# Kernel optimization log

Hardware: AMD Instinct MI355X
Metric: run time of the kernel (lower is better)

The kernel has to match this reference:

```python
import jax, jax.numpy as jnp
import numpy as np
from jax import lax


def _lstm_dir(x, W, U, b, reverse):
    # x: [S, B, in]; W: [4H, in]; U: [4H, H]; b: [4H] (b_ih + b_hh combined)
    if reverse:
        x = x[::-1]
    B = x.shape[1]
    H = U.shape[1]

    def step(carry, xt):
        h, c = carry
        g = xt @ W.T + h @ U.T + b  # [B, 4H], torch gate order i,f,g,o
        i, f, gg, o = jnp.split(g, 4, axis=-1)
        c = jax.nn.sigmoid(f) * c + jax.nn.sigmoid(i) * jnp.tanh(gg)
        h = jax.nn.sigmoid(o) * jnp.tanh(c)
        return (h, c), h

    init = (jnp.zeros((B, H), x.dtype), jnp.zeros((B, H), x.dtype))
    _, hs = lax.scan(step, init, x)
    if reverse:
        hs = hs[::-1]
    return hs  # [S, B, H]


def _bilstm_layer(x, Wih, Whh, b):
    # x: [S, B, in]; Wih: [2, 4H, in]; Whh: [2, 4H, H]; b: [2, 4H]
    fwd = _lstm_dir(x, Wih[0], Whh[0], b[0], False)
    bwd = _lstm_dir(x, Wih[1], Whh[1], b[1], True)
    return jnp.concatenate([fwd, bwd], axis=-1)  # [S, B, 2H]


def _forward(words, chars, emb_table, char_emb_table, char_conv_w, char_conv_b,
             lstm_Wih0, lstm_Whh0, lstm_b0, lstm_Wih1, lstm_Whh1, lstm_b1,
             out_w, out_b):
    B, S = words.shape
    emb = emb_table[words]  # [B, S, E] (dropout = identity in eval)

    # Char CNN: one grouped conv over all B*S positions (replaces the per-position
    # Python loop). NOTE: the original forward discards this (word_features is
    # never used), so it does not affect the returned output -- kept for fidelity.
    ce = char_emb_table[chars]                      # [B, S, W, 25]
    Wl = ce.shape[2]
    x = ce.reshape(B * S, Wl, 25).transpose(0, 2, 1)  # [B*S, 25, W]
    conv = lax.conv_general_dilated(
        x, char_conv_w, (1,), 'VALID',
        dimension_numbers=('NCH', 'OIH', 'NCH'), feature_group_count=25)
    char_feat = jnp.max(conv + char_conv_b[None, :, None], axis=2).reshape(B, S, -1)
    del char_feat  # dead w.r.t. output, exactly as in the original module

    # 2-layer BiLSTM over the word embeddings (all lens == S -> packing is identity)
    h = emb.transpose(1, 0, 2)  # [S, B, E]
    h = _bilstm_layer(h, lstm_Wih0, lstm_Whh0, lstm_b0)
    h = _bilstm_layer(h, lstm_Wih1, lstm_Whh1, lstm_b1)
    lstm_out = h.transpose(1, 0, 2)  # [B, S, 2H]

    # attn_out is computed-but-discarded in the original; output uses lstm_out.
    return jax.nn.sigmoid(lstm_out @ out_w.T + out_b)  # [B, S, n_tags]


def setup_inputs():
    key = jax.random.key(0)
    ks = jax.random.split(key, 14)
    B, S, Wl = 32, 128, 20
    V, E, H, T = 50000, 300, 200, 17
    std = 0.1
    words = jax.random.randint(ks[0], (B, S), 1, V + 2).astype(jnp.int32)
    chars = jax.random.randint(ks[1], (B, S, Wl), 1, 123).astype(jnp.int32)
    lens = jnp.full((B,), S, dtype=jnp.int32)  # full-length sentences
    emb_table = (jax.random.normal(ks[2], (V + 2, E), jnp.float32) * std).at[0].set(0.0)
    char_emb_table = jax.random.normal(ks[3], (123, 25), jnp.float32) * std
    char_conv_w = jax.random.normal(ks[4], (125, 1, 3), jnp.float32) * std  # groups=25
    char_conv_b = jax.random.normal(ks[5], (125,), jnp.float32) * std
    lstm_Wih0 = jax.random.normal(ks[6], (2, 4 * H, E), jnp.float32) * std
    lstm_Whh0 = jax.random.normal(ks[7], (2, 4 * H, H), jnp.float32) * std
    lstm_b0 = jax.random.normal(ks[8], (2, 4 * H), jnp.float32) * std
    lstm_Wih1 = jax.random.normal(ks[9], (2, 4 * H, 2 * H), jnp.float32) * std
    lstm_Whh1 = jax.random.normal(ks[10], (2, 4 * H, H), jnp.float32) * std
    lstm_b1 = jax.random.normal(ks[11], (2, 4 * H), jnp.float32) * std
    out_w = jax.random.normal(ks[12], (T, 2 * H), jnp.float32) * std
    out_b = jax.random.normal(ks[13], (T,), jnp.float32) * std
    return {"words": words, "chars": chars, "lens": lens,
            "emb_table": emb_table, "char_emb_table": char_emb_table,
            "char_conv_w": char_conv_w, "char_conv_b": char_conv_b,
            "lstm_Wih0": lstm_Wih0, "lstm_Whh0": lstm_Whh0, "lstm_b0": lstm_b0,
            "lstm_Wih1": lstm_Wih1, "lstm_Whh1": lstm_Whh1, "lstm_b1": lstm_b1,
            "out_w": out_w, "out_b": out_b}


def reference(words, chars, lens, emb_table, char_emb_table, char_conv_w,
              char_conv_b, lstm_Wih0, lstm_Whh0, lstm_b0, lstm_Wih1, lstm_Whh1,
              lstm_b1, out_w, out_b):
    # lens are all == S, so pack_padded/pad_packed is an identity (no masking).
    return _forward(words, chars, emb_table, char_emb_table, char_conv_w,
                    char_conv_b, lstm_Wih0, lstm_Whh0, lstm_b0,
                    lstm_Wih1, lstm_Whh1, lstm_b1, out_w, out_b)
```

## Files before the change

### kernel.cpp

```cpp
#include <hip/hip_runtime.h>
#include <math.h>

#define SEQ 128
#define BATCH 32
#define EDIM 300
#define HDIM 200
#define G4 800
#define NGATE 1600
#define KC 25
#define NLDS 12
#define CHSTRIDE 6400

#define K0PAD 320
#define K1PAD 416

typedef _Float16 h2t __attribute__((ext_vector_type(2)));
typedef _Float16 f16x8 __attribute__((ext_vector_type(8)));
typedef float f32x4 __attribute__((ext_vector_type(4)));

__device__ __forceinline__ h2t u2h(unsigned v) {
    union { unsigned u; h2t h; } c; c.u = v; return c.h;
}

__device__ __forceinline__ float dot2acc(h2t a, h2t b, float c) {
    return __builtin_amdgcn_fdot2(a, b, c, false);
}

__device__ __forceinline__ float dot8(uint4 u, uint4 h, float acc) {
    acc = dot2acc(u2h(u.x), u2h(h.x), acc);
    acc = dot2acc(u2h(u.y), u2h(h.y), acc);
    acc = dot2acc(u2h(u.z), u2h(h.z), acc);
    acc = dot2acc(u2h(u.w), u2h(h.w), acc);
    return acc;
}

__device__ __forceinline__ float fast_sigmoid(float x) {
    return 1.f / (1.f + __expf(-x));
}
__device__ __forceinline__ float fast_tanh(float x) {
    x = fminf(fmaxf(x, -15.f), 15.f);
    float e = __expf(2.f * x);
    return (e - 1.f) / (e + 1.f);
}

__global__ void k_gather(const int* __restrict__ words,
                         const float* __restrict__ emb,
                         _Float16* __restrict__ X0h)
{
    int row = blockIdx.x;
    int t = row >> 5;
    int b = row & 31;
    int w = words[b * SEQ + t];
    const float* src = emb + (size_t)w * EDIM;
    _Float16* dst = X0h + (size_t)row * K0PAD;
    for (int e = threadIdx.x; e < K0PAD; e += blockDim.x)
        dst[e] = (e < EDIM) ? (_Float16)src[e] : (_Float16)0.f;
}

__global__ void k_castW(const float* __restrict__ W,
                        _Float16* __restrict__ Wh,
                        int N, int K, int Kpad)
{
    int idx = blockIdx.x * blockDim.x + threadIdx.x;
    if (idx >= N * Kpad) return;
    int n = idx / Kpad, k = idx % Kpad;
    Wh[idx] = (k < K) ? (_Float16)W[(size_t)n * K + k] : (_Float16)0.f;
}

__global__ void k_pack(const float* __restrict__ Whh,
                       _Float16* __restrict__ Upk)
{
    int idx = blockIdx.x * blockDim.x + threadIdx.x;
    if (idx >= 2 * KC * 800) return;
    int r  = idx % 800;
    int kc = (idx / 800) % KC;
    int d  = idx / (800 * KC);
    const float* src = Whh + ((size_t)d * G4 + r) * HDIM + kc * 8;
    _Float16* dst = Upk + (size_t)idx * 8;
#pragma unroll
    for (int j = 0; j < 8; ++j) dst[j] = (_Float16)src[j];
}

#define GBM 64
#define GBN 64
#define GBK 32
#define GLD 40

__global__ __launch_bounds__(256)
void k_gemm_mfma(const _Float16* __restrict__ A,
                 const _Float16* __restrict__ Bw,
                 const float* __restrict__ bias,
                 float* __restrict__ C,
                 int M, int N, int Kpad)
{
    __shared__ __align__(16) _Float16 As[GBM][GLD];
    __shared__ __align__(16) _Float16 Bs[GBN][GLD];
    int tid = threadIdx.x;
    int wave = tid >> 6;
    int lane = tid & 63;
    int bm = blockIdx.y * GBM, bn = blockIdx.x * GBN;

    int srow = tid >> 2;
    int sseg = (tid & 3) * 8;

    f32x4 acc0 = {0,0,0,0}, acc1 = {0,0,0,0}, acc2 = {0,0,0,0}, acc3 = {0,0,0,0};
    int am = lane & 15;
    int kg = (lane >> 4) * 8;

    for (int k0 = 0; k0 < Kpad; k0 += GBK) {
        *(f16x8*)&As[srow][sseg] = *(const f16x8*)&A[(size_t)(bm + srow) * Kpad + k0 + sseg];
        *(f16x8*)&Bs[srow][sseg] = *(const f16x8*)&Bw[(size_t)(bn + srow) * Kpad + k0 + sseg];
        __syncthreads();
        f16x8 af = *(const f16x8*)&As[wave * 16 + am][kg];
        f16x8 b0 = *(const f16x8*)&Bs[ 0 + am][kg];
        f16x8 b1 = *(const f16x8*)&Bs[16 + am][kg];
        f16x8 b2 = *(const f16x8*)&Bs[32 + am][kg];
        f16x8 b3 = *(const f16x8*)&Bs[48 + am][kg];
        acc0 = __builtin_amdgcn_mfma_f32_16x16x32_f16(af, b0, acc0, 0, 0, 0);
        acc1 = __builtin_amdgcn_mfma_f32_16x16x32_f16(af, b1, acc1, 0, 0, 0);
        acc2 = __builtin_amdgcn_mfma_f32_16x16x32_f16(af, b2, acc2, 0, 0, 0);
        acc3 = __builtin_amdgcn_mfma_f32_16x16x32_f16(af, b3, acc3, 0, 0, 0);
        __syncthreads();
    }
    int col0 = lane & 15;
    int row0 = (lane >> 4) * 4;
#pragma unroll
    for (int r2 = 0; r2 < 4; ++r2) {
        int m = bm + wave * 16 + row0 + r2;
        float* crow = &C[(size_t)m * N + bn];
        crow[ 0 + col0] = acc0[r2] + bias[bn +  0 + col0];
        crow[16 + col0] = acc1[r2] + bias[bn + 16 + col0];
        crow[32 + col0] = acc2[r2] + bias[bn + 32 + col0];
        crow[48 + col0] = acc3[r2] + bias[bn + 48 + col0];
    }
}

__global__ __launch_bounds__(832)
void k_lstm(const float* __restrict__ Xg,
            const _Float16* __restrict__ Upk,
            float* __restrict__ Hout,
            _Float16* __restrict__ Houth)
{
    int blk = blockIdx.x;
    int d = blk >> 5;
    int b = blk & 31;
    int r = threadIdx.x;
    int rr = (r < G4) ? r : (G4 - 1);

    extern __shared__ __align__(16) char smem[];
    _Float16 (*lds_u)[800][8] = (_Float16 (*)[800][8])smem;
    float* g_lds = (float*)(smem + 153600);
    _Float16 (*hbuf)[HDIM] = (_Float16 (*)[HDIM])(smem + 156800);

    const _Float16* up_ptr = Upk + ((size_t)d * KC * 800 + rr) * 8;

    if (r < G4) {
#pragma unroll
        for (int j = 0; j < NLDS; ++j)
            *(uint4*)&lds_u[j][r][0] =
                *(const uint4*)(up_ptr + (size_t)j * CHSTRIDE);
    }

    if (r < HDIM) hbuf[0][r] = (_Float16)0.f;
    float c = 0.f;

    const float* xg_ptr = Xg + (size_t)b * NGATE + (size_t)d * G4 + rr;
    const ptrdiff_t sstride = (ptrdiff_t)BATCH * NGATE;

    __syncthreads();

    int tt0 = d ? (SEQ - 1) : 0;
    float xg_c = xg_ptr[(ptrdiff_t)tt0 * sstride];

    const _Float16* hcur = hbuf[0];
    _Float16* hnxt = hbuf[1];

#pragma unroll 1
    for (int t = 0; t < SEQ; ++t) {
        int tt = d ? (SEQ - 1 - t) : t;
        float xg_n = 0.f;
        if (t + 1 < SEQ)
            xg_n = xg_ptr[(ptrdiff_t)(d ? (SEQ - 2 - t) : (t + 1)) * sstride];

        float a0 = xg_c, a1 = 0.f;
#pragma unroll
        for (int kc = 0; kc < NLDS; ++kc) {
            uint4 uv = *(const uint4*)&lds_u[kc][rr][0];
            uint4 hv = *(const uint4*)&hcur[8 * kc];
            if (kc & 1) a1 = dot8(uv, hv, a1);
            else        a0 = dot8(uv, hv, a0);
        }
#pragma unroll
        for (int kc = NLDS; kc < KC; ++kc) {
            uint4 uv = *(const uint4*)(up_ptr + (size_t)kc * CHSTRIDE);
            uint4 hv = *(const uint4*)&hcur[8 * kc];
            if (kc & 1) a1 = dot8(uv, hv, a1);
            else        a0 = dot8(uv, hv, a0);
        }
        if (r < G4) g_lds[r] = a0 + a1;
        __syncthreads();

        if (r < HDIM) {
            float gi = g_lds[r];
            float gf = g_lds[HDIM + r];
            float gg = g_lds[2 * HDIM + r];
            float go = g_lds[3 * HDIM + r];
            float si = fast_sigmoid(gi);
            float sf = fast_sigmoid(gf);
            float so = fast_sigmoid(go);
            c = sf * c + si * fast_tanh(gg);
            float hh = so * fast_tanh(c);
            hnxt[r] = (_Float16)hh;
            size_t rowi = (size_t)tt * BATCH + b;
            Hout[rowi * (2 * HDIM) + d * HDIM + r] = hh;
            Houth[rowi * K1PAD + d * HDIM + r] = (_Float16)hh;
        } else if (d == 0 && r >= 800 && r < 816) {
            Houth[((size_t)tt * BATCH + b) * K1PAD + 400 + (r - 800)] = (_Float16)0.f;
        }
        __syncthreads();

        const _Float16* tmp = hcur; hcur = hnxt; hnxt = (_Float16*)tmp;
        xg_c = xg_n;
    }
}

__global__ void k_out(const float* __restrict__ H1,
                      const float* __restrict__ Wo,
                      const float* __restrict__ bo,
                      float* __restrict__ out)
{
    int idx = blockIdx.x * blockDim.x + threadIdx.x;
    if (idx >= BATCH * SEQ * 17) return;
    int o = idx % 17;
    int bs = idx / 17;
    int b = bs >> 7;
    int s = bs & 127;
    const float* hrow = H1 + ((size_t)(s * BATCH + b)) * (2 * HDIM);
    const float* wrow = Wo + (size_t)o * (2 * HDIM);
    float acc = bo[o];
#pragma unroll 4
    for (int j = 0; j < 2 * HDIM; ++j) acc += hrow[j] * wrow[j];
    out[idx] = 1.f / (1.f + __expf(-acc));
}

extern "C" void kernel_launch(void* const* d_in, const int* in_sizes, int n_in,
                              void* d_out, int out_size, void* d_ws, size_t ws_size,
                              hipStream_t stream)
{
    const int*   words = (const int*)d_in[0];
    const float* emb   = (const float*)d_in[3];
    const float* Wih0  = (const float*)d_in[7];
    const float* Whh0  = (const float*)d_in[8];
    const float* b0    = (const float*)d_in[9];
    const float* Wih1  = (const float*)d_in[10];
    const float* Whh1  = (const float*)d_in[11];
    const float* b1    = (const float*)d_in[12];
    const float* Wo    = (const float*)d_in[13];
    const float* bo    = (const float*)d_in[14];
    float* out = (float*)d_out;

    char* ws = (char*)d_ws;
    const size_t X0H_OFF = 0;
    const size_t W0H_OFF = X0H_OFF + (size_t)4096 * K0PAD * 2;
    const size_t W1H_OFF = W0H_OFF + (size_t)NGATE * K0PAD * 2;
    const size_t UP0_OFF = W1H_OFF + (size_t)NGATE * K1PAD * 2;
    const size_t UP1_OFF = UP0_OFF + (size_t)2 * KC * 800 * 8 * 2;
    const size_t XG_OFF  = UP1_OFF + (size_t)2 * KC * 800 * 8 * 2;
    const size_t H1_OFF  = XG_OFF + (size_t)SEQ * BATCH * NGATE * 4;
    const size_t HT0_OFF = H1_OFF + (size_t)SEQ * BATCH * 2 * HDIM * 4;

    _Float16* X0h   = (_Float16*)(ws + X0H_OFF);
    _Float16* W0h   = (_Float16*)(ws + W0H_OFF);
    _Float16* W1h   = (_Float16*)(ws + W1H_OFF);
    _Float16* Upk0  = (_Float16*)(ws + UP0_OFF);
    _Float16* Upk1  = (_Float16*)(ws + UP1_OFF);
    float*    Xg    = (float*)(ws + XG_OFF);
    float*    H1    = (float*)(ws + H1_OFF);
    float*    Hdump = H1;
    _Float16* Houth0 = (_Float16*)(ws + HT0_OFF);
    _Float16* HouthD = Houth0;

    hipFuncSetAttribute((const void*)k_lstm,
                        hipFuncAttributeMaxDynamicSharedMemorySize, 157600);

    k_gather<<<SEQ * BATCH, 128, 0, stream>>>(words, emb, X0h);

    int ncast0 = NGATE * K0PAD, ncast1 = NGATE * K1PAD;
    k_castW<<<(ncast0 + 255) / 256, 256, 0, stream>>>(Wih0, W0h, NGATE, EDIM, K0PAD);
    k_castW<<<(ncast1 + 255) / 256, 256, 0, stream>>>(Wih1, W1h, NGATE, 2 * HDIM, K1PAD);
    int npack = 2 * KC * 800;
    k_pack<<<(npack + 255) / 256, 256, 0, stream>>>(Whh0, Upk0);
    k_pack<<<(npack + 255) / 256, 256, 0, stream>>>(Whh1, Upk1);

    dim3 ggrid(NGATE / GBN, (SEQ * BATCH) / GBM);
    k_gemm_mfma<<<ggrid, 256, 0, stream>>>(X0h, W0h, b0, Xg,
                                           SEQ * BATCH, NGATE, K0PAD);

    k_lstm<<<64, 832, 157600, stream>>>(Xg, Upk0, Hdump, Houth0);

    k_gemm_mfma<<<ggrid, 256, 0, stream>>>(Houth0, W1h, b1, Xg,
                                           SEQ * BATCH, NGATE, K1PAD);

    k_lstm<<<64, 832, 157600, stream>>>(Xg, Upk1, H1, HouthD);

    int nout = BATCH * SEQ * 17;
    k_out<<<(nout + 255) / 256, 256, 0, stream>>>(H1, Wo, bo, out);
}
```

Baseline: 648.6 us.

## Compute all four gates per hidden unit in one thread to drop a barrier

Restructures the recurrent LSTM kernel so that each of 200 worker threads computes the i/f/g/o gate dot products for one hidden unit. The old layout used 800 threads, one per gate row. This removes the g_lds round trip and one __syncthreads per timestep, and shrinks the block to 256 threads. In exchange each thread does four times the dot-product work, so per-step latency rises with longer serial chains. The LDS-resident weight chunks also drop from 12 to 11, which moves more of the U reads to global/L2.

```diff
diff --git a/kernel.cpp b/kernel.cpp
--- a/kernel.cpp
+++ b/kernel.cpp
@@ -8,11 +8,13 @@
 #define G4 800
 #define NGATE 1600
 #define KC 25
-#define NLDS 12
+#define NLDS 11
 #define CHSTRIDE 6400
 
 #define K0PAD 320
 #define K1PAD 416
+
+#define TLSTM 256
 
 typedef _Float16 h2t __attribute__((ext_vector_type(2)));
 typedef _Float16 f16x8 __attribute__((ext_vector_type(8)));
@@ -135,7 +137,7 @@
     }
 }
 
-__global__ __launch_bounds__(832)
+__global__ __launch_bounds__(TLSTM, 1)
 void k_lstm(const float* __restrict__ Xg,
             const _Float16* __restrict__ Upk,
             float* __restrict__ Hout,
@@ -144,33 +146,36 @@
     int blk = blockIdx.x;
     int d = blk >> 5;
     int b = blk & 31;
-    int r = threadIdx.x;
-    int rr = (r < G4) ? r : (G4 - 1);
+    int w = threadIdx.x;
+    bool worker = (w < HDIM);
+    int ww = worker ? w : (HDIM - 1);
 
     extern __shared__ __align__(16) char smem[];
     _Float16 (*lds_u)[800][8] = (_Float16 (*)[800][8])smem;
-    float* g_lds = (float*)(smem + 153600);
-    _Float16 (*hbuf)[HDIM] = (_Float16 (*)[HDIM])(smem + 156800);
-
-    const _Float16* up_ptr = Upk + ((size_t)d * KC * 800 + rr) * 8;
-
-    if (r < G4) {
-#pragma unroll
-        for (int j = 0; j < NLDS; ++j)
-            *(uint4*)&lds_u[j][r][0] =
-                *(const uint4*)(up_ptr + (size_t)j * CHSTRIDE);
-    }
-
-    if (r < HDIM) hbuf[0][r] = (_Float16)0.f;
+    _Float16 (*hbuf)[HDIM] = (_Float16 (*)[HDIM])(smem + 140800);
+
+    for (int idx = w; idx < NLDS * 800; idx += TLSTM) {
+        int kc = idx / 800, r = idx % 800;
+        *(uint4*)&lds_u[kc][r][0] =
+            *(const uint4*)(Upk + ((size_t)(d * KC + kc) * 800 + r) * 8);
+    }
+
+    if (worker) hbuf[0][w] = (_Float16)0.f;
     float c = 0.f;
 
-    const float* xg_ptr = Xg + (size_t)b * NGATE + (size_t)d * G4 + rr;
+    const float* xg_ptr = Xg + (size_t)b * NGATE + (size_t)d * G4 + ww;
     const ptrdiff_t sstride = (ptrdiff_t)BATCH * NGATE;
 
+    const _Float16* upg = Upk + (size_t)d * KC * CHSTRIDE;
+
     __syncthreads();
 
     int tt0 = d ? (SEQ - 1) : 0;
-    float xg_c = xg_ptr[(ptrdiff_t)tt0 * sstride];
+    float xI_c = 0.f, xF_c = 0.f, xG_c = 0.f, xO_c = 0.f;
+    if (worker) {
+        const float* p = xg_ptr + (ptrdiff_t)tt0 * sstride;
+        xI_c = p[0]; xF_c = p[HDIM]; xG_c = p[2*HDIM]; xO_c = p[3*HDIM];
+    }
 
     const _Float16* hcur = hbuf[0];
     _Float16* hnxt = hbuf[1];
@@ -178,49 +183,56 @@
 #pragma unroll 1
     for (int t = 0; t < SEQ; ++t) {
         int tt = d ? (SEQ - 1 - t) : t;
-        float xg_n = 0.f;
-        if (t + 1 < SEQ)
-            xg_n = xg_ptr[(ptrdiff_t)(d ? (SEQ - 2 - t) : (t + 1)) * sstride];
-
-        float a0 = xg_c, a1 = 0.f;
+        float xI_n = 0.f, xF_n = 0.f, xG_n = 0.f, xO_n = 0.f;
+        if (worker && t + 1 < SEQ) {
+            const float* p = xg_ptr + (ptrdiff_t)(d ? (SEQ-2-t) : (t+1)) * sstride;
+            xI_n = p[0]; xF_n = p[HDIM]; xG_n = p[2*HDIM]; xO_n = p[3*HDIM];
+        }
+
+        float aI = xI_c, aF = xF_c, aG = xG_c, aO = xO_c;
 #pragma unroll
         for (int kc = 0; kc < NLDS; ++kc) {
-            uint4 uv = *(const uint4*)&lds_u[kc][rr][0];
             uint4 hv = *(const uint4*)&hcur[8 * kc];
-            if (kc & 1) a1 = dot8(uv, hv, a1);
-            else        a0 = dot8(uv, hv, a0);
+            uint4 uI = *(const uint4*)&lds_u[kc][ww          ][0];
+            uint4 uF = *(const uint4*)&lds_u[kc][ww + HDIM   ][0];
+            uint4 uG = *(const uint4*)&lds_u[kc][ww + 2*HDIM ][0];
+            uint4 uO = *(const uint4*)&lds_u[kc][ww + 3*HDIM ][0];
+            aI = dot8(uI, hv, aI);
+            aF = dot8(uF, hv, aF);
+            aG = dot8(uG, hv, aG);
+            aO = dot8(uO, hv, aO);
         }
 #pragma unroll
         for (int kc = NLDS; kc < KC; ++kc) {
-            uint4 uv = *(const uint4*)(up_ptr + (size_t)kc * CHSTRIDE);
             uint4 hv = *(const uint4*)&hcur[8 * kc];
-            if (kc & 1) a1 = dot8(uv, hv, a1);
-            else        a0 = dot8(uv, hv, a0);
+            const _Float16* base = upg + (size_t)kc * CHSTRIDE;
+            uint4 uI = *(const uint4*)(base + (ww          ) * 8);
+            uint4 uF = *(const uint4*)(base + (ww + HDIM   ) * 8);
+            uint4 uG = *(const uint4*)(base + (ww + 2*HDIM ) * 8);
+            uint4 uO = *(const uint4*)(base + (ww + 3*HDIM ) * 8);
+            aI = dot8(uI, hv, aI);
+            aF = dot8(uF, hv, aF);
+            aG = dot8(uG, hv, aG);
+            aO = dot8(uO, hv, aO);
         }
-        if (r < G4) g_lds[r] = a0 + a1;
-        __syncthreads();
-
-        if (r < HDIM) {
-            float gi = g_lds[r];
-            float gf = g_lds[HDIM + r];
-            float gg = g_lds[2 * HDIM + r];
-            float go = g_lds[3 * HDIM + r];
-            float si = fast_sigmoid(gi);
-            float sf = fast_sigmoid(gf);
-            float so = fast_sigmoid(go);
-            c = sf * c + si * fast_tanh(gg);
+
+        if (worker) {
+            float si = fast_sigmoid(aI);
+            float sf = fast_sigmoid(aF);
+            float so = fast_sigmoid(aO);
+            c = sf * c + si * fast_tanh(aG);
             float hh = so * fast_tanh(c);
-            hnxt[r] = (_Float16)hh;
+            hnxt[w] = (_Float16)hh;
             size_t rowi = (size_t)tt * BATCH + b;
-            Hout[rowi * (2 * HDIM) + d * HDIM + r] = hh;
-            Houth[rowi * K1PAD + d * HDIM + r] = (_Float16)hh;
-        } else if (d == 0 && r >= 800 && r < 816) {
-            Houth[((size_t)tt * BATCH + b) * K1PAD + 400 + (r - 800)] = (_Float16)0.f;
+            Hout[rowi * (2 * HDIM) + d * HDIM + w] = hh;
+            Houth[rowi * K1PAD + d * HDIM + w] = (_Float16)hh;
+        } else if (d == 0 && w >= HDIM && w < HDIM + 16) {
+            Houth[((size_t)tt * BATCH + b) * K1PAD + 400 + (w - HDIM)] = (_Float16)0.f;
         }
         __syncthreads();
 
         const _Float16* tmp = hcur; hcur = hnxt; hnxt = (_Float16*)tmp;
-        xg_c = xg_n;
+        xI_c = xI_n; xF_c = xF_n; xG_c = xG_n; xO_c = xO_n;
     }
 }
 
@@ -281,7 +293,7 @@
     _Float16* HouthD = Houth0;
 
     hipFuncSetAttribute((const void*)k_lstm,
-                        hipFuncAttributeMaxDynamicSharedMemorySize, 157600);
+                        hipFuncAttributeMaxDynamicSharedMemorySize, 141600);
 
     k_gather<<<SEQ * BATCH, 128, 0, stream>>>(words, emb, X0h);
 
@@ -296,12 +308,12 @@
     k_gemm_mfma<<<ggrid, 256, 0, stream>>>(X0h, W0h, b0, Xg,
                                            SEQ * BATCH, NGATE, K0PAD);
 
-    k_lstm<<<64, 832, 157600, stream>>>(Xg, Upk0, Hdump, Houth0);
+    k_lstm<<<64, TLSTM, 141600, stream>>>(Xg, Upk0, Hdump, Houth0);
 
     k_gemm_mfma<<<ggrid, 256, 0, stream>>>(Houth0, W1h, b1, Xg,
                                            SEQ * BATCH, NGATE, K1PAD);
 
-    k_lstm<<<64, 832, 157600, stream>>>(Xg, Upk1, H1, HouthD);
+    k_lstm<<<64, TLSTM, 141600, stream>>>(Xg, Upk1, H1, HouthD);
 
     int nout = BATCH * SEQ * 17;
     k_out<<<(nout + 255) / 256, 256, 0, stream>>>(H1, Wo, bo, out);
```

New measurement: 2.106 ms. 225% more time.
